# Kernel tuning notes

Hardware: AMD Instinct MI355X
Metric: run time of the kernel (lower is better)

## Reference

```python
import jax, jax.numpy as jnp
import numpy as np

D_MODEL = 1024
N_HEADS = 16
N_GROUPS = 4
HEAD_DIM = D_MODEL // N_HEADS          # 64
HPG = N_HEADS // N_GROUPS              # heads per group = 4
KV_DIM = N_GROUPS * HEAD_DIM           # 256


def setup_inputs() -> dict:
    key = jax.random.key(0)
    ks = jax.random.split(key, 9)
    B, T = 2, 2048
    s = 0.02
    return {
        "x":  jax.random.normal(ks[0], (B, T, D_MODEL), dtype=jnp.float32),
        "Wq": jax.random.normal(ks[1], (D_MODEL, D_MODEL), dtype=jnp.float32) * s,
        "bq": jnp.zeros((D_MODEL,), dtype=jnp.float32),
        "Wk": jax.random.normal(ks[2], (D_MODEL, KV_DIM), dtype=jnp.float32) * s,
        "bk": jnp.zeros((KV_DIM,), dtype=jnp.float32),
        "Wv": jax.random.normal(ks[3], (D_MODEL, KV_DIM), dtype=jnp.float32) * s,
        "bv": jnp.zeros((KV_DIM,), dtype=jnp.float32),
        "Wo": jax.random.normal(ks[4], (D_MODEL, D_MODEL), dtype=jnp.float32) * s,
        "bo": jnp.zeros((D_MODEL,), dtype=jnp.float32),
    }


def reference(x, Wq, bq, Wk, bk, Wv, bv, Wo, bo):
    B, T, C = x.shape
    q = x @ Wq + bq                                   # [B,T,C]
    k = x @ Wk + bk                                   # [B,T,G*hd]
    v = x @ Wv + bv

    # [B, G, hpg, T, hd] for q; [B, G, T, hd] for k,v (native GQA head sharing,
    # equivalent to repeat_interleave on the group dim in the torch code)
    q = q.reshape(B, T, N_GROUPS, HPG, HEAD_DIM).transpose(0, 2, 3, 1, 4)
    k = k.reshape(B, T, N_GROUPS, HEAD_DIM).transpose(0, 2, 1, 3)
    v = v.reshape(B, T, N_GROUPS, HEAD_DIM).transpose(0, 2, 1, 3)

    scale = 1.0 / jnp.sqrt(jnp.float32(HEAD_DIM))
    attn = jnp.einsum('bghqd,bgkd->bghqk', q, k) * scale   # [B,G,hpg,T,T]

    causal = jnp.tril(jnp.ones((T, T), dtype=bool))        # True = keep
    attn = jnp.where(causal, attn, jnp.float32(-jnp.inf))
    attn = jax.nn.softmax(attn, axis=-1)
    # dropout p=0.1 only in training mode; reference is eval mode (identity)

    out = jnp.einsum('bghqk,bgkd->bghqd', attn, v)         # [B,G,hpg,T,hd]
    out = out.transpose(0, 3, 1, 2, 4).reshape(B, T, C)
    return out @ Wo + bo
```

## Files before the change

kernel.cpp:

```cpp
#include <hip/hip_runtime.h>
#include <hip/hip_bf16.h>
#include <stdint.h>

#define D_MODEL 1024
#define T_LEN   2048
#define BATCH   2
#define N_HEADS 16
#define KV_DIM  256
#define QKV_N   1536
#define M_ROWS  (BATCH * T_LEN)

typedef unsigned short u16;
typedef __bf16 bf16x8 __attribute__((ext_vector_type(8)));
typedef __bf16 bf16x2 __attribute__((ext_vector_type(2)));
typedef float  f32x4  __attribute__((ext_vector_type(4)));

__device__ __forceinline__ u16 f2b(float f) {
    uint32_t u = __builtin_bit_cast(uint32_t, f);
    u += 0x7FFFu + ((u >> 16) & 1u);
    return (u16)(u >> 16);
}

__device__ __forceinline__ uint32_t pk_bf16(float a, float b) {
#if __has_builtin(__builtin_amdgcn_cvt_pk_bf16_f32)
    bf16x2 v = __builtin_amdgcn_cvt_pk_bf16_f32(a, b);
    return __builtin_bit_cast(uint32_t, v);
#else
    return (uint32_t)f2b(a) | ((uint32_t)f2b(b) << 16);
#endif
}

__device__ __forceinline__ void gl_lds16(const void* g, void* l) {
    __builtin_amdgcn_global_load_lds(g, l, 16, 0, 0);
}

__global__ __launch_bounds__(256) void prep(
    const float* __restrict__ x,
    const float* __restrict__ Wq, const float* __restrict__ Wk,
    const float* __restrict__ Wv, const float* __restrict__ Wo,
    u16* __restrict__ xb, u16* __restrict__ WcatT, u16* __restrict__ WoT)
{
    __shared__ u16 tile[32][33];
    int id = blockIdx.x;
    int tid = threadIdx.x;
    if (id < 2048) {
        int i = (id * 256 + tid) * 8;
        float4 a = *(const float4*)&x[i];
        float4 c = *(const float4*)&x[i + 4];
        u16 r[8] = { f2b(a.x), f2b(a.y), f2b(a.z), f2b(a.w),
                     f2b(c.x), f2b(c.y), f2b(c.z), f2b(c.w) };
        *(uint4*)&xb[i] = *(const uint4*)r;
        return;
    }
    int t = id - 2048;
    int bx = t % 80;
    int k0 = (t / 80) * 32;
    const float* src; u16* dst; int N, n0;
    if (bx < 32)       { src = Wq; dst = WcatT;                   N = 1024; n0 = bx * 32; }
    else if (bx < 40)  { src = Wk; dst = WcatT + 1024 * 1024;     N = 256;  n0 = (bx - 32) * 32; }
    else if (bx < 48)  { src = Wv; dst = WcatT + 1280 * 1024;     N = 256;  n0 = (bx - 40) * 32; }
    else               { src = Wo; dst = WoT;                     N = 1024; n0 = (bx - 48) * 32; }
    for (int i = 0; i < 4; ++i) {
        int idx = tid + i * 256;
        int r = idx >> 5, c = idx & 31;
        tile[r][c] = f2b(src[(size_t)(k0 + r) * N + (n0 + c)]);
    }
    __syncthreads();
    for (int i = 0; i < 4; ++i) {
        int idx = tid + i * 256;
        int r = idx >> 5, c = idx & 31;
        dst[(size_t)(n0 + r) * 1024 + (k0 + c)] = tile[c][r];
    }
}

__global__ __launch_bounds__(256) void gemm_qkv(
    const u16* __restrict__ A, const u16* __restrict__ BT,
    const float* __restrict__ bq, const float* __restrict__ bk,
    const float* __restrict__ bv, u16* __restrict__ Qb,
    u16* __restrict__ Kpack, u16* __restrict__ Vpack)
{
    constexpr int K = 1024;
    constexpr float SCALE = 0.125f * 1.44269504088896f;
    __shared__ __align__(16) u16 As[64 * 64];
    __shared__ __align__(16) u16 Bs[128 * 64];

    int tid  = threadIdx.x;
    int lane = tid & 63, w = tid >> 6;
    int quad = lane >> 4, l15 = lane & 15;
    int m0 = blockIdx.y * 64, n0 = blockIdx.x * 128;
    int lr = lane >> 3, lc = (lane & 7) * 8;

    f32x4 acc[4][2] = {};

    for (int k0 = 0; k0 < K; k0 += 64) {
        for (int t = 0; t < 2; ++t) {
            int rb = t * 32 + w * 8;
            gl_lds16(&A[(size_t)(m0 + rb + lr) * K + k0 + lc], &As[rb * 64]);
        }
        for (int t = 0; t < 4; ++t) {
            int rb = t * 32 + w * 8;
            gl_lds16(&BT[(size_t)(n0 + rb + lr) * K + k0 + lc], &Bs[rb * 64]);
        }
        __syncthreads();
        for (int kk = 0; kk < 64; kk += 32) {
            bf16x8 a[4], b[2];
            for (int i = 0; i < 4; ++i)
                a[i] = *(const bf16x8*)&As[(i * 16 + l15) * 64 + kk + quad * 8];
            for (int j = 0; j < 2; ++j)
                b[j] = *(const bf16x8*)&Bs[(w * 32 + j * 16 + l15) * 64 + kk + quad * 8];
            for (int i = 0; i < 4; ++i)
                for (int j = 0; j < 2; ++j)
                    acc[i][j] = __builtin_amdgcn_mfma_f32_16x16x32_bf16(
                        a[i], b[j], acc[i][j], 0, 0, 0);
        }
        __syncthreads();
    }

    for (int j = 0; j < 2; ++j) {
        int col = n0 + w * 32 + j * 16 + l15;
        float bj = (col < 1024) ? bq[col] : (col < 1280) ? bk[col - 1024] : bv[col - 1280];
        for (int i = 0; i < 4; ++i) {
            int rowb = m0 + i * 16 + quad * 4;
            int bb = rowb >> 11, keyloc = rowb & 2047;
            int t64 = keyloc >> 6;
            if (col < 1024) {
                for (int r = 0; r < 4; ++r)
                    Qb[(size_t)(rowb + r) * 1024 + col] =
                        f2b((acc[i][j][r] + bj) * SCALE);
            } else if (col < 1280) {
                int d = col - 1024; int g = d >> 6; d &= 63;
                int kk = d >> 5, qd = (d >> 3) & 3, e = d & 7;
                int ntk = (keyloc >> 4) & 3, l15k = keyloc & 15;
                size_t base = ((((size_t)(bb * 4 + g) * 32 + t64) * 2 + kk) * 4
                               + ntk) * 512 + qd * 128 + l15k * 8 + e;
                for (int r = 0; r < 4; ++r)
                    Kpack[base + r * 8] = f2b(acc[i][j][r] + bj);
            } else {
                int d = col - 1280; int g = d >> 6; d &= 63;
                int dt = d >> 4, l15v = d & 15;
                int kkp = (keyloc >> 5) & 1, qv = (keyloc >> 3) & 3, e0 = keyloc & 7;
                u16 tmp[4];
                for (int r = 0; r < 4; ++r) tmp[r] = f2b(acc[i][j][r] + bj);
                size_t base = ((((size_t)(bb * 4 + g) * 32 + t64) * 2 + kkp) * 4
                               + dt) * 512 + (qv * 16 + l15v) * 8 + e0;
                *(uint64_t*)&Vpack[base] = *(const uint64_t*)tmp;
            }
        }
    }
}

__global__ __launch_bounds__(256) void gemm_out(
    const u16* __restrict__ A, const u16* __restrict__ BT,
    const float* __restrict__ bias, float* __restrict__ C)
{
    constexpr int K = 1024, N = 1024;
    __shared__ __align__(16) u16 As[64 * 64];
    __shared__ __align__(16) u16 Bs[128 * 64];

    int tid  = threadIdx.x;
    int lane = tid & 63, w = tid >> 6;
    int quad = lane >> 4, l15 = lane & 15;
    int m0 = blockIdx.y * 64, n0 = blockIdx.x * 128;
    int lr = lane >> 3, lc = (lane & 7) * 8;

    f32x4 acc[4][2] = {};

    for (int k0 = 0; k0 < K; k0 += 64) {
        for (int t = 0; t < 2; ++t) {
            int rb = t * 32 + w * 8;
            gl_lds16(&A[(size_t)(m0 + rb + lr) * K + k0 + lc], &As[rb * 64]);
        }
        for (int t = 0; t < 4; ++t) {
            int rb = t * 32 + w * 8;
            gl_lds16(&BT[(size_t)(n0 + rb + lr) * K + k0 + lc], &Bs[rb * 64]);
        }
        __syncthreads();
        for (int kk = 0; kk < 64; kk += 32) {
            bf16x8 a[4], b[2];
            for (int i = 0; i < 4; ++i)
                a[i] = *(const bf16x8*)&As[(i * 16 + l15) * 64 + kk + quad * 8];
            for (int j = 0; j < 2; ++j)
                b[j] = *(const bf16x8*)&Bs[(w * 32 + j * 16 + l15) * 64 + kk + quad * 8];
            for (int i = 0; i < 4; ++i)
                for (int j = 0; j < 2; ++j)
                    acc[i][j] = __builtin_amdgcn_mfma_f32_16x16x32_bf16(
                        a[i], b[j], acc[i][j], 0, 0, 0);
        }
        __syncthreads();
    }

    for (int j = 0; j < 2; ++j) {
        int col = n0 + w * 32 + j * 16 + l15;
        float bj = bias[col];
        for (int i = 0; i < 4; ++i) {
            int rowb = m0 + i * 16 + quad * 4;
            for (int r = 0; r < 4; ++r)
                C[(size_t)(rowb + r) * N + col] = acc[i][j][r] + bj;
        }
    }
}

__global__ __launch_bounds__(256, 4) void attn_kernel(
    const u16* __restrict__ Qb,
    const u16* __restrict__ Kpack,
    const u16* __restrict__ Vpack,
    u16* __restrict__ AO)
{
    constexpr int LDP = 72;
    __shared__ __align__(16) u16 Kv[4096];
    __shared__ __align__(16) u16 Vv[4096];
    __shared__ __align__(16) u16 Ps[4][16 * LDP];

    int tid  = threadIdx.x;
    int lane = tid & 63, w = tid >> 6;
    int quad = lane >> 4, l15 = lane & 15;

    int gid = blockIdx.x;
    int b = gid & 1, g = (gid >> 1) & 3;
    int s = gid >> 3;
    int kq = s >> 5, tq = s & 31;
    int q4 = (kq & 1) ? tq : (31 - tq);
    int j  = q4 * 4 + kq;
    int head = g * 4 + w;
    int q0 = j * 16;
    int iters = q4 + 1;

    const u16* Qp = Qb + ((size_t)b * T_LEN + q0) * 1024 + head * 64;
    const u16* Kp = Kpack + (size_t)(b * 4 + g) * 131072;
    const u16* Vp = Vpack + (size_t)(b * 4 + g) * 131072;
    u16*       Op = AO + ((size_t)b * T_LEN + q0) * D_MODEL + head * 64;
    u16* Pw = Ps[w];

    bf16x8 Qfrag[2];
    #pragma unroll
    for (int kk = 0; kk < 2; ++kk)
        Qfrag[kk] = *(const bf16x8*)&Qp[(size_t)l15 * 1024 + kk * 32 + quad * 8];

    f32x4 o[4] = {};
    float lsum = 0.f;

    for (int tg = 0; tg < iters; ++tg) {
        bool diag = (tg == iters - 1);

        const u16* kt = Kp + (size_t)tg * 4096;
        const u16* vt = Vp + (size_t)tg * 4096;
        #pragma unroll
        for (int c = 0; c < 2; ++c) {
            int ch = w * 2 + c;
            gl_lds16(kt + ch * 512 + lane * 8, &Kv[ch * 512]);
            gl_lds16(vt + ch * 512 + lane * 8, &Vv[ch * 512]);
        }
        __syncthreads();

        f32x4 sacc[4] = {};
        #pragma unroll
        for (int kk = 0; kk < 2; ++kk) {
            bf16x8 bQ = Qfrag[kk];
            #pragma unroll
            for (int ntk = 0; ntk < 4; ++ntk) {
                bf16x8 aK = *(const bf16x8*)&Kv[(kk * 4 + ntk) * 512 + lane * 8];
                sacc[ntk] = __builtin_amdgcn_mfma_f32_16x16x32_bf16(
                    aK, bQ, sacc[ntk], 0, 0, 0);
            }
        }
        int qrow = q0 + l15;
        float lacc = 0.f;
        #pragma unroll
        for (int ntk = 0; ntk < 4; ++ntk) {
            float p0, p1, p2, p3;
            if (diag) {
                int key = tg * 64 + ntk * 16 + quad * 4;
                p0 = (key + 0 <= qrow) ? exp2f(sacc[ntk][0]) : 0.f;
                p1 = (key + 1 <= qrow) ? exp2f(sacc[ntk][1]) : 0.f;
                p2 = (key + 2 <= qrow) ? exp2f(sacc[ntk][2]) : 0.f;
                p3 = (key + 3 <= qrow) ? exp2f(sacc[ntk][3]) : 0.f;
            } else {
                p0 = exp2f(sacc[ntk][0]);
                p1 = exp2f(sacc[ntk][1]);
                p2 = exp2f(sacc[ntk][2]);
                p3 = exp2f(sacc[ntk][3]);
            }
            lacc += (p0 + p1) + (p2 + p3);
            uint2 pv;
            pv.x = pk_bf16(p0, p1);
            pv.y = pk_bf16(p2, p3);
            *(uint2*)&Pw[l15 * LDP + ntk * 16 + quad * 4] = pv;
        }
        lsum += lacc;

        #pragma unroll
        for (int kkp = 0; kkp < 2; ++kkp) {
            bf16x8 aP = *(const bf16x8*)&Pw[l15 * LDP + kkp * 32 + quad * 8];
            #pragma unroll
            for (int dt = 0; dt < 4; ++dt) {
                bf16x8 bV = *(const bf16x8*)&Vv[(kkp * 4 + dt) * 512 + lane * 8];
                o[dt] = __builtin_amdgcn_mfma_f32_16x16x32_bf16(
                    aP, bV, o[dt], 0, 0, 0);
            }
        }
        __syncthreads();
    }

    float l = lsum;
    l += __shfl_xor(l, 16, 64);
    l += __shfl_xor(l, 32, 64);
    float linv = 1.0f / l;
    float li[4];
    #pragma unroll
    for (int r = 0; r < 4; ++r)
        li[r] = __shfl(linv, quad * 4 + r, 64);
    #pragma unroll
    for (int dt = 0; dt < 4; ++dt)
        #pragma unroll
        for (int r = 0; r < 4; ++r)
            Op[(size_t)(quad * 4 + r) * D_MODEL + dt * 16 + l15] =
                f2b(o[dt][r] * li[r]);
}

extern "C" void kernel_launch(void* const* d_in, const int* in_sizes, int n_in,
                              void* d_out, int out_size, void* d_ws, size_t ws_size,
                              hipStream_t stream) {
    const float* x  = (const float*)d_in[0];
    const float* Wq = (const float*)d_in[1];
    const float* bq = (const float*)d_in[2];
    const float* Wk = (const float*)d_in[3];
    const float* bk = (const float*)d_in[4];
    const float* Wv = (const float*)d_in[5];
    const float* bv = (const float*)d_in[6];
    const float* Wo = (const float*)d_in[7];
    const float* bo = (const float*)d_in[8];
    float* out = (float*)d_out;

    u16* ws    = (u16*)d_ws;
    u16* xb    = ws;  ws += (size_t)M_ROWS * 1024;
    u16* WcatT = ws;  ws += (size_t)QKV_N * 1024;
    u16* WoT   = ws;  ws += 1024 * 1024;
    u16* Qb    = ws;  ws += (size_t)M_ROWS * 1024;
    u16* Kpack = ws;  ws += (size_t)M_ROWS * KV_DIM;
    u16* Vpack = ws;  ws += (size_t)M_ROWS * KV_DIM;
    u16* AO    = xb;

    prep<<<2048 + 2560, 256, 0, stream>>>(x, Wq, Wk, Wv, Wo, xb, WcatT, WoT);
    gemm_qkv<<<dim3(QKV_N / 128, M_ROWS / 64), 256, 0, stream>>>(
        xb, WcatT, bq, bk, bv, Qb, Kpack, Vpack);
    attn_kernel<<<1024, 256, 0, stream>>>(Qb, Kpack, Vpack, AO);
    gemm_out<<<dim3(1024 / 128, M_ROWS / 64), 256, 0, stream>>>(AO, WoT, bo, out);
}
```

Baseline: 177.8 us.

## Split long causal attention rows into two KV halves with LPT scheduling and combine

Query tiles with many key blocks (q4>=16) are split into two blocks over halves of the KV range, each writing unnormalized fp32 partial outputs and row sums to workspace. A separate combine kernel adds the partials and normalizes them into AO. A constant table orders the blocks in a longest-processing-time sequence, and launch bounds are raised to 6 waves per SIMD. The aim is to balance work across CUs and cut the tail of the causal attention. The cost is an extra kernel launch plus fp32 partial traffic to and from workspace. Skipping the running max in the softmax is safe here because the two halves share no max subtraction, so their plain exp sums add directly.

```diff
diff --git a/kernel.cpp b/kernel.cpp
--- a/kernel.cpp
+++ b/kernel.cpp
@@ -33,6 +33,15 @@
 __device__ __forceinline__ void gl_lds16(const void* g, void* l) {
     __builtin_amdgcn_global_load_lds(g, l, 16, 0, 0);
 }
+
+__constant__ unsigned char LPT_TBL[48] = {
+    62, 63, 60, 15, 61, 58, 59, 56,
+    50, 53, 13, 52, 55, 54, 57, 14,
+    51, 48, 12, 49, 46, 47, 44, 11,
+    39, 38, 41, 10, 40, 43, 42, 45,
+    36,  9, 37, 34, 35, 32,  8, 33,
+     0,  1,  2,  3,  4,  5,  6,  7
+};
 
 __global__ __launch_bounds__(256) void prep(
     const float* __restrict__ x,
@@ -200,11 +209,13 @@
     }
 }
 
-__global__ __launch_bounds__(256, 4) void attn_kernel(
+__global__ __launch_bounds__(256, 6) void attn_kernel(
     const u16* __restrict__ Qb,
     const u16* __restrict__ Kpack,
     const u16* __restrict__ Vpack,
-    u16* __restrict__ AO)
+    u16* __restrict__ AO,
+    float* __restrict__ Opart,
+    float* __restrict__ Lpart)
 {
     constexpr int LDP = 72;
     __shared__ __align__(16) u16 Kv[4096];
@@ -216,18 +227,29 @@
     int quad = lane >> 4, l15 = lane & 15;
 
     int gid = blockIdx.x;
-    int b = gid & 1, g = (gid >> 1) & 3;
-    int s = gid >> 3;
-    int kq = s >> 5, tq = s & 31;
-    int q4 = (kq & 1) ? tq : (31 - tq);
-    int j  = q4 * 4 + kq;
+    int bg = gid & 7;
+    int b = bg >> 2, g = bg & 3;
+    int idx = gid >> 3;
+    int code = LPT_TBL[idx >> 2];
+    int kq = idx & 3;
+    int q4, h = 0, tgB, tgE;
+    bool split;
+    if (code < 32) {
+        split = false; q4 = code; tgB = 0; tgE = q4 + 1;
+    } else {
+        split = true; q4 = code >> 1; h = code & 1;
+        int nA = (q4 + 2) >> 1;
+        tgB = h ? nA : 0;
+        tgE = h ? (q4 + 1) : nA;
+    }
+    int j = q4 * 4 + kq;
     int head = g * 4 + w;
     int q0 = j * 16;
-    int iters = q4 + 1;
+    int iters64 = q4 + 1;
 
     const u16* Qp = Qb + ((size_t)b * T_LEN + q0) * 1024 + head * 64;
-    const u16* Kp = Kpack + (size_t)(b * 4 + g) * 131072;
-    const u16* Vp = Vpack + (size_t)(b * 4 + g) * 131072;
+    const u16* Kp = Kpack + (size_t)bg * 131072;
+    const u16* Vp = Vpack + (size_t)bg * 131072;
     u16*       Op = AO + ((size_t)b * T_LEN + q0) * D_MODEL + head * 64;
     u16* Pw = Ps[w];
 
@@ -238,9 +260,10 @@
 
     f32x4 o[4] = {};
     float lsum = 0.f;
-
-    for (int tg = 0; tg < iters; ++tg) {
-        bool diag = (tg == iters - 1);
+    int qrow = q0 + l15;
+
+    for (int tg = tgB; tg < tgE; ++tg) {
+        bool diag = (tg == iters64 - 1);
 
         const u16* kt = Kp + (size_t)tg * 4096;
         const u16* vt = Vp + (size_t)tg * 4096;
@@ -263,7 +286,6 @@
                     aK, bQ, sacc[ntk], 0, 0, 0);
             }
         }
-        int qrow = q0 + l15;
         float lacc = 0.f;
         #pragma unroll
         for (int ntk = 0; ntk < 4; ++ntk) {
@@ -304,17 +326,64 @@
     float l = lsum;
     l += __shfl_xor(l, 16, 64);
     l += __shfl_xor(l, 32, 64);
-    float linv = 1.0f / l;
-    float li[4];
-    #pragma unroll
-    for (int r = 0; r < 4; ++r)
-        li[r] = __shfl(linv, quad * 4 + r, 64);
-    #pragma unroll
-    for (int dt = 0; dt < 4; ++dt)
+
+    if (!split) {
+        float linv = 1.0f / l;
+        float li[4];
         #pragma unroll
         for (int r = 0; r < 4; ++r)
-            Op[(size_t)(quad * 4 + r) * D_MODEL + dt * 16 + l15] =
-                f2b(o[dt][r] * li[r]);
+            li[r] = __shfl(linv, quad * 4 + r, 64);
+        #pragma unroll
+        for (int dt = 0; dt < 4; ++dt)
+            #pragma unroll
+            for (int r = 0; r < 4; ++r)
+                Op[(size_t)(quad * 4 + r) * D_MODEL + dt * 16 + l15] =
+                    f2b(o[dt][r] * li[r]);
+    } else {
+        int p = ((bg * 16 + (q4 - 16)) * 4 + kq) * 2 + h;
+        size_t obase = (size_t)(p * 4 + w) * 1024;
+        #pragma unroll
+        for (int dt = 0; dt < 4; ++dt)
+            #pragma unroll
+            for (int r = 0; r < 4; ++r)
+                Opart[obase + (size_t)(quad * 4 + r) * 64 + dt * 16 + l15] =
+                    o[dt][r];
+        if (quad == 0)
+            Lpart[(size_t)(p * 4 + w) * 16 + l15] = l;
+    }
+}
+
+__global__ __launch_bounds__(64) void attn_combine(
+    const float* __restrict__ Opart, const float* __restrict__ Lpart,
+    u16* __restrict__ AO)
+{
+    int gid = blockIdx.x;
+    int w  = gid & 3;
+    int sp = gid >> 2;
+    int bg = sp >> 6;
+    int rest = sp & 63;
+    int q4 = 16 + (rest >> 2);
+    int kq = rest & 3;
+    int b = bg >> 2, g = bg & 3;
+    int head = g * 4 + w;
+    int j = q4 * 4 + kq;
+    int q0 = j * 16;
+    int pA = ((bg * 16 + (q4 - 16)) * 4 + kq) * 2;
+
+    const float* OA = Opart + (size_t)(pA * 4 + w) * 1024;
+    const float* OB = Opart + (size_t)((pA + 1) * 4 + w) * 1024;
+    const float* LA = Lpart + (size_t)(pA * 4 + w) * 16;
+    const float* LB = Lpart + (size_t)((pA + 1) * 4 + w) * 16;
+
+    int d = threadIdx.x;
+    #pragma unroll 4
+    for (int row = 0; row < 16; ++row) {
+        float l = LA[row] + LB[row];
+        float linv = 1.0f / l;
+        float v = OA[row * 64 + d] + OB[row * 64 + d];
+        AO[((size_t)(b * T_LEN + q0 + row)) * D_MODEL + head * 64 + d] =
+            f2b(v * linv);
+    }
 }
 
 extern "C" void kernel_launch(void* const* d_in, const int* in_sizes, int n_in,
@@ -338,11 +407,14 @@
     u16* Qb    = ws;  ws += (size_t)M_ROWS * 1024;
     u16* Kpack = ws;  ws += (size_t)M_ROWS * KV_DIM;
     u16* Vpack = ws;  ws += (size_t)M_ROWS * KV_DIM;
+    float* Opart = (float*)ws;
+    float* Lpart = Opart + (size_t)1024 * 4 * 1024;
     u16* AO    = xb;
 
     prep<<<2048 + 2560, 256, 0, stream>>>(x, Wq, Wk, Wv, Wo, xb, WcatT, WoT);
     gemm_qkv<<<dim3(QKV_N / 128, M_ROWS / 64), 256, 0, stream>>>(
         xb, WcatT, bq, bk, bv, Qb, Kpack, Vpack);
-    attn_kernel<<<1024, 256, 0, stream>>>(Qb, Kpack, Vpack, AO);
+    attn_kernel<<<1536, 256, 0, stream>>>(Qb, Kpack, Vpack, AO, Opart, Lpart);
+    attn_combine<<<2048, 64, 0, stream>>>(Opart, Lpart, AO);
     gemm_out<<<dim3(1024 / 128, M_ROWS / 64), 256, 0, stream>>>(AO, WoT, bo, out);
 }
```

Result: no change. 175.1 us (-1.5%).
